# Kernel tuning notes

Hardware: AMD Instinct MI355X
Metric: run time of the kernel (lower is better)

Reference implementation:

```python
import jax, jax.numpy as jnp
import numpy as np

TEMPERATURE = 0.07
EPS_NORM = 1e-12  # F.normalize eps

def _l2_normalize(x):
    # matches torch.nn.functional.normalize(dim=1): x / max(||x||, eps)
    norm = jnp.linalg.norm(x, axis=1, keepdims=True)
    return x / jnp.maximum(norm, EPS_NORM)

def setup_inputs() -> dict:
    key = jax.random.key(0)
    k1, k2, k3, k4 = jax.random.split(key, 4)
    N, M, D, C = 8192, 8192, 1024, 128
    return {
        "features_a": jax.random.normal(k1, (N, D), dtype=jnp.float32),
        "features_b": jax.random.normal(k2, (M, D), dtype=jnp.float32),
        "labels_a": jax.random.randint(k3, (N,), 0, C, dtype=jnp.int64),
        "labels_b": jax.random.randint(k4, (M,), 0, C, dtype=jnp.int64),
    }

def reference(features_a, features_b, labels_a, labels_b):
    fa = _l2_normalize(features_a)
    fb = _l2_normalize(features_b)
    sim = jnp.matmul(fa, fb.T) / TEMPERATURE          # [N, M]
    sim = jnp.clip(sim, -50.0, 50.0)
    exp_sim = jnp.exp(sim)
    positive_mask = (labels_a[:, None] == labels_b[None, :]).astype(exp_sim.dtype)
    pos_sum = jnp.sum(exp_sim * positive_mask, axis=1, keepdims=True)
    neg_sum = jnp.sum(exp_sim, axis=1, keepdims=True)
    pos_sum = jnp.maximum(pos_sum, 1e-8)
    loss = -jnp.mean(jnp.log(pos_sum / neg_sum))
    return loss
```

## Files before the change

### kernel.cpp

```cpp
#include <hip/hip_runtime.h>
#include <hip/hip_bf16.h>
#include <math.h>

typedef __attribute__((ext_vector_type(4))) float f32x4;
typedef __attribute__((ext_vector_type(16))) float f32x16;
typedef __attribute__((ext_vector_type(8))) int i32x8;
typedef __attribute__((ext_vector_type(4))) int i32x4;

#define TEMP_INV 14.2857142857142857f
#define SCALE_EPI 0.013950892857142857f
#define UNIT_SCALE 0x7f7f7f7f

union frag32 {
  i32x8 v8;
  struct { i32x4 lo; i32x4 hi; } s;
};

static __device__ inline void async16(const void* g, void* l) {
  __builtin_amdgcn_global_load_lds(
      (const __attribute__((address_space(1))) unsigned int*)g,
      (__attribute__((address_space(3))) unsigned int*)l,
      16, 0, 0);
}

static __device__ inline int fp4e(float y) {
  const float af = fabsf(y);
  int code = (af > 0.25f) + (af > 0.75f) + (af > 1.25f) + (af > 1.75f) +
             (af > 2.5f) + (af > 3.5f) + (af > 5.0f);
  return code | (y < 0.f ? 8 : 0);
}


__global__ __launch_bounds__(1024) void normalize_rows(
    const float* __restrict__ a, const float* __restrict__ b,
    int* __restrict__ oa, int* __restrict__ ob,
    float* __restrict__ pos_acc, float* __restrict__ neg_acc,
    float* __restrict__ dout, int N, int D) {
  __shared__ __align__(16) unsigned short sPk[8192];

  const int blk = blockIdx.x;
  const bool isA = blk < 256;
  const int p = isA ? blk : blk - 256;
  const float* src = (isA ? a : b) + (size_t)p * 32 * D;
  int* out = isA ? oa : ob;

  const int tid = threadIdx.x;
  const int r = tid >> 5;
  const int c = tid & 31;

  if (blk == 0 && tid == 0) dout[0] = 0.f;
  if (isA && c == 0) {
    pos_acc[p * 32 + r] = 0.f;
    neg_acc[p * 32 + r] = 0.f;
  }

  const float4* inr = (const float4*)(src + (size_t)r * D);
  float4 v[8];
#pragma unroll
  for (int i = 0; i < 8; i++) v[i] = inr[c + 32 * i];

  float ss = 0.f;
#pragma unroll
  for (int i = 0; i < 8; i++)
    ss += v[i].x * v[i].x + v[i].y * v[i].y + v[i].z * v[i].z + v[i].w * v[i].w;
#pragma unroll
  for (int m = 16; m >= 1; m >>= 1) ss += __shfl_xor(ss, m, 32);
  const float inv = 32.0f / fmaxf(sqrtf(ss), 1e-12f);

#pragma unroll
  for (int i = 0; i < 8; i++) {
    const int f = c + 32 * i;
    const int n0 = fp4e(v[i].x * inv);
    const int n1 = fp4e(v[i].y * inv);
    const int n2 = fp4e(v[i].z * inv);
    const int n3 = fp4e(v[i].w * inv);
    const unsigned short h =
        (unsigned short)(n0 | (n1 << 4) | (n2 << 8) | (n3 << 12));
    const int s = f >> 4;
    const int hi = (f >> 3) & 1;
    sPk[s * 512 + (hi * 32 + r) * 8 + (f & 7)] = h;
  }
  __syncthreads();

  const int4* sp4 = (const int4*)sPk;
  ((int4*)out)[(size_t)p * 1024 + tid] = sp4[tid];
}

__global__ __launch_bounds__(256, 4) void infonce_gemm(
    const unsigned char* __restrict__ A, const unsigned char* __restrict__ B,
    const int* __restrict__ la, const int* __restrict__ lb,
    float* __restrict__ pos_acc, float* __restrict__ neg_acc) {
  __shared__ __align__(16) unsigned char sA[16384];
  __shared__ __align__(16) unsigned char sB[16384];

  const int tid = threadIdx.x;
  const int lane = tid & 63;
  const int wave = tid >> 6;
  const int wa = wave >> 1;
  const int wb = wave & 1;

  const int bid = blockIdx.x;
  const int xcd = bid & 7;
  const int local = bid >> 3;
  const int by = xcd * 8 + (local & 7);
  const int bx = local >> 3;
  const int row0 = by * 128;
  const int col0 = bx * 128;

  const unsigned char* gA =
      A + (size_t)by * 65536 + ((tid >> 6) & 3) * 1024 + (tid & 63) * 16;
  const unsigned char* gB =
      B + (size_t)bx * 65536 + ((tid >> 6) & 3) * 1024 + (tid & 63) * 16;

  f32x16 acc[2][2] = {};

#define STAGE(kt)                                                   \
  do {                                                              \
    _Pragma("unroll") for (int u = 0; u < 4; u++) {                 \
      async16(gA + (size_t)u * 16384 + (size_t)(kt)*4096,           \
              &sA[u * 4096 + tid * 16]);                            \
      async16(gB + (size_t)u * 16384 + (size_t)(kt)*4096,           \
              &sB[u * 4096 + tid * 16]);                            \
    }                                                               \
  } while (0)

#define LD16(dst, base, off)                                        \
  do {                                                              \
    frag32 _f;                                                      \
    _f.s.lo = *(const i32x4*)((base) + (off));                      \
    _f.s.hi = (i32x4){0, 0, 0, 0};                                  \
    dst = _f.v8;                                                    \
  } while (0)

#define MFMA(ci, x_, y_)                                            \
  ci = __builtin_amdgcn_mfma_scale_f32_32x32x64_f8f6f4(             \
      x_, y_, ci, 4, 4, 0, UNIT_SCALE, 0, UNIT_SCALE)

  const int lofs = lane * 16;
  const int aoff0 = (wa * 2 + 0) * 4096 + lofs;
  const int aoff1 = (wa * 2 + 1) * 4096 + lofs;
  const int boff0 = (wb * 2 + 0) * 4096 + lofs;
  const int boff1 = (wb * 2 + 1) * 4096 + lofs;

#pragma unroll 1
  for (int kt = 0; kt < 4; ++kt) {
    STAGE(kt);
    __syncthreads();
#pragma unroll
    for (int sp = 0; sp < 4; ++sp) {
      i32x8 fa0, fa1, fb0, fb1;
      LD16(fa0, sA, aoff0 + sp * 1024);
      LD16(fa1, sA, aoff1 + sp * 1024);
      LD16(fb0, sB, boff0 + sp * 1024);
      LD16(fb1, sB, boff1 + sp * 1024);
      MFMA(acc[0][0], fb0, fa0);
      MFMA(acc[0][1], fb0, fa1);
      MFMA(acc[1][0], fb1, fa0);
      MFMA(acc[1][1], fb1, fa1);
    }
    __syncthreads();
  }

  const int l31 = lane & 31;
  const int hi = lane >> 5;
  const int colw = col0 + wb * 64 + 4 * hi;
  const int rowbase = row0 + wa * 64 + l31;

  const int lav0 = la[rowbase];
  const int lav1 = la[rowbase + 32];

  int lbs[2][16];
#pragma unroll
  for (int bi = 0; bi < 2; bi++)
#pragma unroll
    for (int r = 0; r < 16; r++)
      lbs[bi][r] = lb[colw + bi * 32 + (r & 3) + 8 * (r >> 2)];

#pragma unroll
  for (int aj = 0; aj < 2; aj++) {
    const int lav = aj ? lav1 : lav0;
    float sn = 0.f, sp = 0.f;
#pragma unroll
    for (int bi = 0; bi < 2; bi++)
#pragma unroll
      for (int r = 0; r < 16; r++) {
        const float e = __expf(acc[bi][aj][r] * SCALE_EPI);
        sn += e;
        sp += (lav == lbs[bi][r]) ? e : 0.f;
      }
    sn += __shfl_xor(sn, 32, 64);
    sp += __shfl_xor(sp, 32, 64);
    if (hi == 0) {
      const int row = rowbase + aj * 32;
      atomicAdd(&neg_acc[row], sn);
      atomicAdd(&pos_acc[row], sp);
    }
  }
}

__global__ __launch_bounds__(256) void final_reduce(
    const float* __restrict__ pos, const float* __restrict__ neg,
    float* __restrict__ out, int N) {
  const int i = blockIdx.x * 256 + threadIdx.x;
  const float4 p4 = ((const float4*)pos)[i];
  const float4 n4 = ((const float4*)neg)[i];
  float local = (logf(n4.x) - logf(fmaxf(p4.x, 1e-8f))) +
                (logf(n4.y) - logf(fmaxf(p4.y, 1e-8f))) +
                (logf(n4.z) - logf(fmaxf(p4.z, 1e-8f))) +
                (logf(n4.w) - logf(fmaxf(p4.w, 1e-8f)));
#pragma unroll
  for (int m = 32; m >= 1; m >>= 1) local += __shfl_xor(local, m, 64);
  __shared__ float ws[4];
  const int wv = threadIdx.x >> 6, lane = threadIdx.x & 63;
  if (lane == 0) ws[wv] = local;
  __syncthreads();
  if (threadIdx.x == 0)
    atomicAdd(out, (ws[0] + ws[1] + ws[2] + ws[3]) * (1.0f / (float)N));
}

extern "C" void kernel_launch(void* const* d_in, const int* in_sizes, int n_in,
                              void* d_out, int out_size, void* d_ws, size_t ws_size,
                              hipStream_t stream) {
  const float* fa = (const float*)d_in[0];
  const float* fb = (const float*)d_in[1];
  const int* la = (const int*)d_in[2];
  const int* lb = (const int*)d_in[3];

  const int D = 1024;
  const int N = in_sizes[0] / D;
  const int M = in_sizes[1] / D;

  unsigned char* nA = (unsigned char*)d_ws;
  unsigned char* nB = nA + (size_t)N * D / 2;
  float* pos = (float*)(nB + (size_t)M * D / 2);
  float* neg = pos + N;

  normalize_rows<<<512, 1024, 0, stream>>>(fa, fb, (int*)nA, (int*)nB, pos,
                                           neg, (float*)d_out, N, D);

  infonce_gemm<<<4096, 256, 0, stream>>>(nA, nB, la, lb, pos, neg);

  final_reduce<<<8, 256, 0, stream>>>(pos, neg, (float*)d_out, N);
}
```

Before: 148.1 us.

## Fuse normalize, GEMM and reduction into one cooperative persistent kernel

```diff
diff --git a/kernel.cpp b/kernel.cpp
--- a/kernel.cpp
+++ b/kernel.cpp
@@ -1,6 +1,9 @@
 #include <hip/hip_runtime.h>
+#include <hip/hip_cooperative_groups.h>
 #include <hip/hip_bf16.h>
 #include <math.h>
+
+namespace cg = cooperative_groups;
 
 typedef __attribute__((ext_vector_type(4))) float f32x4;
 typedef __attribute__((ext_vector_type(16))) float f32x16;
@@ -31,88 +34,101 @@
 }
 
 
-__global__ __launch_bounds__(1024) void normalize_rows(
+__global__ __launch_bounds__(256, 4) void fused_all(
     const float* __restrict__ a, const float* __restrict__ b,
-    int* __restrict__ oa, int* __restrict__ ob,
+    unsigned char* __restrict__ oa, unsigned char* __restrict__ ob,
+    const int* __restrict__ la, const int* __restrict__ lb,
     float* __restrict__ pos_acc, float* __restrict__ neg_acc,
-    float* __restrict__ dout, int N, int D) {
-  __shared__ __align__(16) unsigned short sPk[8192];
-
-  const int blk = blockIdx.x;
-  const bool isA = blk < 256;
-  const int p = isA ? blk : blk - 256;
-  const float* src = (isA ? a : b) + (size_t)p * 32 * D;
-  int* out = isA ? oa : ob;
-
-  const int tid = threadIdx.x;
-  const int r = tid >> 5;
-  const int c = tid & 31;
-
-  if (blk == 0 && tid == 0) dout[0] = 0.f;
-  if (isA && c == 0) {
-    pos_acc[p * 32 + r] = 0.f;
-    neg_acc[p * 32 + r] = 0.f;
-  }
-
-  const float4* inr = (const float4*)(src + (size_t)r * D);
-  float4 v[8];
-#pragma unroll
-  for (int i = 0; i < 8; i++) v[i] = inr[c + 32 * i];
-
-  float ss = 0.f;
-#pragma unroll
-  for (int i = 0; i < 8; i++)
-    ss += v[i].x * v[i].x + v[i].y * v[i].y + v[i].z * v[i].z + v[i].w * v[i].w;
-#pragma unroll
-  for (int m = 16; m >= 1; m >>= 1) ss += __shfl_xor(ss, m, 32);
-  const float inv = 32.0f / fmaxf(sqrtf(ss), 1e-12f);
-
-#pragma unroll
-  for (int i = 0; i < 8; i++) {
-    const int f = c + 32 * i;
-    const int n0 = fp4e(v[i].x * inv);
-    const int n1 = fp4e(v[i].y * inv);
-    const int n2 = fp4e(v[i].z * inv);
-    const int n3 = fp4e(v[i].w * inv);
-    const unsigned short h =
-        (unsigned short)(n0 | (n1 << 4) | (n2 << 8) | (n3 << 12));
-    const int s = f >> 4;
-    const int hi = (f >> 3) & 1;
-    sPk[s * 512 + (hi * 32 + r) * 8 + (f & 7)] = h;
-  }
-  __syncthreads();
-
-  const int4* sp4 = (const int4*)sPk;
-  ((int4*)out)[(size_t)p * 1024 + tid] = sp4[tid];
-}
-
-__global__ __launch_bounds__(256, 4) void infonce_gemm(
-    const unsigned char* __restrict__ A, const unsigned char* __restrict__ B,
-    const int* __restrict__ la, const int* __restrict__ lb,
-    float* __restrict__ pos_acc, float* __restrict__ neg_acc) {
+    float* __restrict__ dout) {
   __shared__ __align__(16) unsigned char sA[16384];
   __shared__ __align__(16) unsigned char sB[16384];
 
   const int tid = threadIdx.x;
-  const int lane = tid & 63;
-  const int wave = tid >> 6;
-  const int wa = wave >> 1;
-  const int wb = wave & 1;
-
   const int bid = blockIdx.x;
-  const int xcd = bid & 7;
-  const int local = bid >> 3;
-  const int by = xcd * 8 + (local & 7);
-  const int bx = local >> 3;
-  const int row0 = by * 128;
-  const int col0 = bx * 128;
-
-  const unsigned char* gA =
-      A + (size_t)by * 65536 + ((tid >> 6) & 3) * 1024 + (tid & 63) * 16;
-  const unsigned char* gB =
-      B + (size_t)bx * 65536 + ((tid >> 6) & 3) * 1024 + (tid & 63) * 16;
-
-  f32x16 acc[2][2] = {};
+
+  {
+    const int pg = bid >> 1;
+    const int sub = bid & 1;
+    const bool isA = pg < 256;
+    const int p = isA ? pg : pg - 256;
+    const float* src = (isA ? a : b) + ((size_t)p * 32 + sub * 16) * 1024;
+    int4* out4 = (int4*)(isA ? oa : ob);
+
+    const int r16 = tid >> 4;
+    const int c16 = tid & 15;
+    if (bid == 0 && tid == 0) dout[0] = 0.f;
+    if (isA && tid < 16) {
+      const int row = p * 32 + sub * 16 + tid;
+      pos_acc[row] = 0.f;
+      neg_acc[row] = 0.f;
+    }
+
+    const float4* inr = (const float4*)(src + (size_t)r16 * 1024);
+    float4 v[16];
+#pragma unroll
+    for (int i = 0; i < 16; i++) v[i] = inr[c16 + 16 * i];
+    float ss = 0.f;
+#pragma unroll
+    for (int i = 0; i < 16; i++)
+      ss += v[i].x * v[i].x + v[i].y * v[i].y + v[i].z * v[i].z +
+            v[i].w * v[i].w;
+#pragma unroll
+    for (int m = 8; m >= 1; m >>= 1) ss += __shfl_xor(ss, m, 16);
+    const float inv = 32.0f / fmaxf(sqrtf(ss), 1e-12f);
+
+    unsigned short* pk = (unsigned short*)sA;
+    const int hi_ = (c16 >> 3) & 1;
+    const int j_ = c16 & 7;
+#pragma unroll
+    for (int i = 0; i < 16; i++) {
+      const int n0 = fp4e(v[i].x * inv);
+      const int n1 = fp4e(v[i].y * inv);
+      const int n2 = fp4e(v[i].z * inv);
+      const int n3 = fp4e(v[i].w * inv);
+      const unsigned short h =
+          (unsigned short)(n0 | (n1 << 4) | (n2 << 8) | (n3 << 12));
+      pk[i * 256 + hi_ * 128 + r16 * 8 + j_] = h;
+    }
+    __syncthreads();
+    const int4* sp4 = (const int4*)pk;
+#pragma unroll
+    for (int w = 0; w < 2; w++) {
+      const int v4 = tid + 256 * w;
+      const int i = v4 >> 5;
+      const int hi2 = (v4 >> 4) & 1;
+      out4[(size_t)(p * 16 + i) * 64 + hi2 * 32 + sub * 16 + (v4 & 15)] =
+          sp4[v4];
+    }
+    __syncthreads();
+  }
+
+  cg::this_grid().sync();
+
+  {
+    const int lane = tid & 63;
+    const int wave = tid >> 6;
+    const int wa = wave >> 1;
+    const int wb = wave & 1;
+    const int xcd = bid & 7;
+    const int local = bid >> 3;
+    const int by = xcd * 8 + (local & 7);
+    const int bxg = local >> 3;
+    const int row0 = by * 128;
+
+    const int sr1k = ((tid >> 6) & 3) * 1024 + (tid & 63) * 16;
+    const unsigned char* gA = oa + (size_t)by * 65536 + sr1k;
+
+    const int lofs = lane * 16;
+    const int aoff0 = (wa * 2 + 0) * 4096 + lofs;
+    const int aoff1 = (wa * 2 + 1) * 4096 + lofs;
+    const int boff0 = (wb * 2 + 0) * 4096 + lofs;
+    const int boff1 = (wb * 2 + 1) * 4096 + lofs;
+
+    const int l31 = lane & 31;
+    const int hi = lane >> 5;
+    const int rowbase = row0 + wa * 64 + l31;
+    const int lav0 = la[rowbase];
+    const int lav1 = la[rowbase + 32];
 
 #define STAGE(kt)                                                   \
   do {                                                              \
@@ -136,12 +152,156 @@
   ci = __builtin_amdgcn_mfma_scale_f32_32x32x64_f8f6f4(             \
       x_, y_, ci, 4, 4, 0, UNIT_SCALE, 0, UNIT_SCALE)
 
+#pragma unroll 1
+    for (int t = 0; t < 4; ++t) {
+      const int bx = bxg * 4 + t;
+      const int col0 = bx * 128;
+      const unsigned char* gB = ob + (size_t)bx * 65536 + sr1k;
+
+      f32x16 acc[2][2] = {};
+
+#pragma unroll 1
+      for (int kt = 0; kt < 4; ++kt) {
+        STAGE(kt);
+        __syncthreads();
+#pragma unroll
+        for (int sp = 0; sp < 4; ++sp) {
+          i32x8 fa0, fa1, fb0, fb1;
+          LD16(fa0, sA, aoff0 + sp * 1024);
+          LD16(fa1, sA, aoff1 + sp * 1024);
+          LD16(fb0, sB, boff0 + sp * 1024);
+          LD16(fb1, sB, boff1 + sp * 1024);
+          MFMA(acc[0][0], fb0, fa0);
+          MFMA(acc[0][1], fb0, fa1);
+          MFMA(acc[1][0], fb1, fa0);
+          MFMA(acc[1][1], fb1, fa1);
+        }
+        __syncthreads();
+      }
+
+      const int colw = col0 + wb * 64 + 4 * hi;
+      int lbs[2][16];
+#pragma unroll
+      for (int bi = 0; bi < 2; bi++)
+#pragma unroll
+        for (int r = 0; r < 16; r++)
+          lbs[bi][r] = lb[colw + bi * 32 + (r & 3) + 8 * (r >> 2)];
+
+#pragma unroll
+      for (int aj = 0; aj < 2; aj++) {
+        const int lav = aj ? lav1 : lav0;
+        float sn = 0.f, sp = 0.f;
+#pragma unroll
+        for (int bi = 0; bi < 2; bi++)
+#pragma unroll
+          for (int r = 0; r < 16; r++) {
+            const float e = __expf(acc[bi][aj][r] * SCALE_EPI);
+            sn += e;
+            sp += (lav == lbs[bi][r]) ? e : 0.f;
+          }
+        sn += __shfl_xor(sn, 32, 64);
+        sp += __shfl_xor(sp, 32, 64);
+        if (hi == 0) {
+          const int row = rowbase + aj * 32;
+          atomicAdd(&neg_acc[row], sn);
+          atomicAdd(&pos_acc[row], sp);
+        }
+      }
+    }
+  }
+
+  cg::this_grid().sync();
+
+  if (bid < 8) {
+    const int i = bid * 256 + tid;
+    const float4 p4 = ((const float4*)pos_acc)[i];
+    const float4 n4 = ((const float4*)neg_acc)[i];
+    float local = (logf(n4.x) - logf(fmaxf(p4.x, 1e-8f))) +
+                  (logf(n4.y) - logf(fmaxf(p4.y, 1e-8f))) +
+                  (logf(n4.z) - logf(fmaxf(p4.z, 1e-8f))) +
+                  (logf(n4.w) - logf(fmaxf(p4.w, 1e-8f)));
+#pragma unroll
+    for (int m = 32; m >= 1; m >>= 1) local += __shfl_xor(local, m, 64);
+    __shared__ float ws[4];
+    const int wv = tid >> 6, lane = tid & 63;
+    if (lane == 0) ws[wv] = local;
+    __syncthreads();
+    if (tid == 0)
+      atomicAdd(dout, (ws[0] + ws[1] + ws[2] + ws[3]) * (1.0f / 8192.0f));
+  }
+}
+
+__global__ __launch_bounds__(1024) void normalize_rows(
+    const float* __restrict__ a, const float* __restrict__ b,
+    int* __restrict__ oa, int* __restrict__ ob,
+    float* __restrict__ pos_acc, float* __restrict__ neg_acc,
+    float* __restrict__ dout, int N, int D) {
+  __shared__ __align__(16) unsigned short sPk[8192];
+  const int blk = blockIdx.x;
+  const bool isA = blk < 256;
+  const int p = isA ? blk : blk - 256;
+  const float* src = (isA ? a : b) + (size_t)p * 32 * D;
+  int* out = isA ? oa : ob;
+  const int tid = threadIdx.x;
+  const int r = tid >> 5, c = tid & 31;
+  if (blk == 0 && tid == 0) dout[0] = 0.f;
+  if (isA && c == 0) {
+    pos_acc[p * 32 + r] = 0.f;
+    neg_acc[p * 32 + r] = 0.f;
+  }
+  const float4* inr = (const float4*)(src + (size_t)r * D);
+  float4 v[8];
+#pragma unroll
+  for (int i = 0; i < 8; i++) v[i] = inr[c + 32 * i];
+  float ss = 0.f;
+#pragma unroll
+  for (int i = 0; i < 8; i++)
+    ss += v[i].x * v[i].x + v[i].y * v[i].y + v[i].z * v[i].z + v[i].w * v[i].w;
+#pragma unroll
+  for (int m = 16; m >= 1; m >>= 1) ss += __shfl_xor(ss, m, 32);
+  const float inv = 32.0f / fmaxf(sqrtf(ss), 1e-12f);
+#pragma unroll
+  for (int i = 0; i < 8; i++) {
+    const int n0 = fp4e(v[i].x * inv);
+    const int n1 = fp4e(v[i].y * inv);
+    const int n2 = fp4e(v[i].z * inv);
+    const int n3 = fp4e(v[i].w * inv);
+    const unsigned short h =
+        (unsigned short)(n0 | (n1 << 4) | (n2 << 8) | (n3 << 12));
+    const int f = c + 32 * i;
+    sPk[(f >> 4) * 512 + (((f >> 3) & 1) * 32 + r) * 8 + (f & 7)] = h;
+  }
+  __syncthreads();
+  const int4* sp4 = (const int4*)sPk;
+  int4* op4 = (int4*)(out + (size_t)p * 2048);
+#pragma unroll
+  for (int j = 0; j < 1; j++) op4[tid] = sp4[tid];
+}
+
+__global__ __launch_bounds__(256, 4) void infonce_gemm(
+    const unsigned char* __restrict__ A, const unsigned char* __restrict__ B,
+    const int* __restrict__ la, const int* __restrict__ lb,
+    float* __restrict__ pos_acc, float* __restrict__ neg_acc) {
+  __shared__ __align__(16) unsigned char sA[16384];
+  __shared__ __align__(16) unsigned char sB[16384];
+  const int tid = threadIdx.x;
+  const int lane = tid & 63;
+  const int wave = tid >> 6;
+  const int wa = wave >> 1, wb = wave & 1;
+  const int bid = blockIdx.x;
+  const int xcd = bid & 7, local = bid >> 3;
+  const int by = xcd * 8 + (local & 7);
+  const int bx = local >> 3;
+  const int row0 = by * 128, col0 = bx * 128;
+  const int sr1k = ((tid >> 6) & 3) * 1024 + (tid & 63) * 16;
+  const unsigned char* gA = A + (size_t)by * 65536 + sr1k;
+  const unsigned char* gB = B + (size_t)bx * 65536 + sr1k;
+  f32x16 acc[2][2] = {};
   const int lofs = lane * 16;
   const int aoff0 = (wa * 2 + 0) * 4096 + lofs;
   const int aoff1 = (wa * 2 + 1) * 4096 + lofs;
   const int boff0 = (wb * 2 + 0) * 4096 + lofs;
   const int boff1 = (wb * 2 + 1) * 4096 + lofs;
-
 #pragma unroll 1
   for (int kt = 0; kt < 4; ++kt) {
     STAGE(kt);
@@ -160,22 +320,18 @@
     }
     __syncthreads();
   }
-
   const int l31 = lane & 31;
   const int hi = lane >> 5;
   const int colw = col0 + wb * 64 + 4 * hi;
   const int rowbase = row0 + wa * 64 + l31;
-
   const int lav0 = la[rowbase];
   const int lav1 = la[rowbase + 32];
-
   int lbs[2][16];
 #pragma unroll
   for (int bi = 0; bi < 2; bi++)
 #pragma unroll
     for (int r = 0; r < 16; r++)
       lbs[bi][r] = lb[colw + bi * 32 + (r & 3) + 8 * (r >> 2)];
-
 #pragma unroll
   for (int aj = 0; aj < 2; aj++) {
     const int lav = aj ? lav1 : lav0;
@@ -234,11 +390,18 @@
   unsigned char* nB = nA + (size_t)N * D / 2;
   float* pos = (float*)(nB + (size_t)M * D / 2);
   float* neg = pos + N;
-
-  normalize_rows<<<512, 1024, 0, stream>>>(fa, fb, (int*)nA, (int*)nB, pos,
-                                           neg, (float*)d_out, N, D);
-
-  infonce_gemm<<<4096, 256, 0, stream>>>(nA, nB, la, lb, pos, neg);
-
-  final_reduce<<<8, 256, 0, stream>>>(pos, neg, (float*)d_out, N);
-}
+  float* outp = (float*)d_out;
+
+  void* args[] = {(void*)&fa, (void*)&fb, (void*)&nA, (void*)&nB,
+                  (void*)&la, (void*)&lb, (void*)&pos, (void*)&neg,
+                  (void*)&outp};
+  hipError_t err = hipLaunchCooperativeKernel(
+      (const void*)fused_all, dim3(1024), dim3(256), args, 0, stream);
+  if (err != hipSuccess) {
+    (void)hipGetLastError();
+    normalize_rows<<<512, 1024, 0, stream>>>(fa, fb, (int*)nA, (int*)nB, pos,
+                                             neg, outp, N, D);
+    infonce_gemm<<<4096, 256, 0, stream>>>(nA, nB, la, lb, pos, neg);
+    final_reduce<<<8, 256, 0, stream>>>(pos, neg, outp, N);
+  }
+}
```

Result: slower. 372.1 us (+151.3%).
